# Performance work log

Hardware: AMD Instinct MI355X
Metric: run time of the kernel (lower is better)

## Reference

```python
import jax, jax.numpy as jnp
import numpy as np

EM_DIM = 64
GROUP = 16
DIM_IN = 1024


def _position_embedding(boxes, part_boxes):
    # boxes: [N,4], part_boxes: [P,4] -> [N,P,EM_DIM]
    xmin, ymin, xmax, ymax = [boxes[:, i:i + 1] for i in range(4)]            # [N,1]
    pxmin, pymin, pxmax, pymax = [part_boxes[:, i:i + 1].T for i in range(4)]  # [1,P]
    bw = xmax - xmin + 1.0
    bh = ymax - ymin + 1.0
    pw = pxmax - pxmin + 1.0
    ph = pymax - pymin + 1.0
    cx = 0.5 * (xmin + xmax)
    cy = 0.5 * (ymin + ymax)
    pcx = 0.5 * (pxmin + pxmax)
    pcy = 0.5 * (pymin + pymax)
    dx = jnp.abs((cx - pcx) / bw)
    dy = jnp.abs((cy - pcy) / bh)
    dx = jnp.log(jnp.where(dx < 1e-3, 1e-3, dx))
    dy = jnp.log(jnp.where(dy < 1e-3, 1e-3, dy))
    dw = jnp.log(pw / bw)
    dh = jnp.log(ph / bh)
    pos = jnp.stack([dx, dy, dw, dh], axis=2)                                  # [N,P,4]
    em_range = jnp.arange(EM_DIM // 8, dtype=pos.dtype) / (EM_DIM // 8)        # [8]
    em_mat = jnp.power(jnp.asarray(1000.0, pos.dtype), em_range)               # [8]
    div = (100.0 * pos)[..., None] / em_mat                                    # [N,P,4,8]
    emb = jnp.concatenate([jnp.sin(div), jnp.cos(div)], axis=3)                # [N,P,4,16]
    return emb.reshape(pos.shape[0], pos.shape[1], EM_DIM)


def _single_relation(boxes, part_boxes, bf, pf, Wg_w, Wg_b, Wq_w, Wq_b, Wk_w, Wk_b, conv_w, conv_b):
    N = bf.shape[0]
    P = pf.shape[0]
    emb = _position_embedding(boxes, part_boxes)                               # [N,P,64]
    pos_feat = jax.nn.relu(emb @ Wg_w.T + Wg_b)                                # [N,P,G]
    att_weight = jnp.transpose(pos_feat, (0, 2, 1))                            # [N,G,P]
    q = (bf @ Wq_w.T + Wq_b).reshape(N, GROUP, EM_DIM)                         # [N,G,64]
    k = (pf @ Wk_w.T + Wk_b).reshape(P, GROUP, EM_DIM)                         # [P,G,64]
    att = jnp.einsum('ngd,pgd->ngp', q, k) * (1.0 / GROUP)                     # [N,G,P]
    att_weight = jnp.where(att_weight < 1e-6, 1e-6, att_weight)
    sm = jax.nn.softmax(jnp.log(att_weight) + att, axis=2)                     # [N,G,P]
    out = jnp.einsum('ngp,pc->ngc', sm, pf)                                    # [N,G,dim_in]
    # grouped 1x1 conv: group g maps dim_in channels -> EM_DIM channels
    w3 = conv_w.reshape(GROUP, EM_DIM, DIM_IN)
    rel = jnp.einsum('ngc,goc->ngo', out, w3).reshape(N, GROUP * EM_DIM) + conv_b
    return rel                                                                  # [N, G*EM_DIM]


def setup_inputs() -> dict:
    key = jax.random.key(0)
    ks = jax.random.split(key, 12)
    N_TOT, P_TOT = 2048, 2048

    def make_rois(k1, k2, n, n1):
        xy = jax.random.uniform(k1, (n, 2), jnp.float32) * 800.0
        wh = jax.random.uniform(k2, (n, 2), jnp.float32) * 200.0 + 16.0
        boxes = jnp.concatenate([xy, xy + wh], axis=1)
        idx = jnp.concatenate([jnp.zeros((n1, 1)), jnp.ones((n - n1, 1))], axis=0).astype(jnp.float32)
        return jnp.concatenate([idx, boxes], axis=1)

    rois = make_rois(ks[0], ks[1], N_TOT, 1024)
    part_rois = make_rois(ks[2], ks[3], P_TOT, 1024)
    box_feats = jax.random.normal(ks[4], (N_TOT, DIM_IN), jnp.float32)
    part_feats = jax.random.normal(ks[5], (P_TOT, DIM_IN), jnp.float32)
    xav_g = float(np.sqrt(6.0 / (EM_DIM + GROUP)))
    xav_qk = float(np.sqrt(6.0 / (DIM_IN + GROUP * EM_DIM)))
    Wg_w = jax.random.uniform(ks[6], (GROUP, EM_DIM), jnp.float32, -xav_g, xav_g)
    Wg_b = jnp.zeros((GROUP,), jnp.float32)
    Wq_w = jax.random.uniform(ks[7], (GROUP * EM_DIM, DIM_IN), jnp.float32, -xav_qk, xav_qk)
    Wq_b = jnp.zeros((GROUP * EM_DIM,), jnp.float32)
    Wk_w = jax.random.uniform(ks[8], (GROUP * EM_DIM, DIM_IN), jnp.float32, -xav_qk, xav_qk)
    Wk_b = jnp.zeros((GROUP * EM_DIM,), jnp.float32)
    conv_w = jax.random.normal(ks[9], (GROUP * EM_DIM, DIM_IN), jnp.float32) * 0.02
    conv_b = jnp.zeros((GROUP * EM_DIM,), jnp.float32)
    return {"rois": rois, "part_rois": part_rois, "box_feats": box_feats,
            "part_feats": part_feats, "Wg_w": Wg_w, "Wg_b": Wg_b,
            "Wq_w": Wq_w, "Wq_b": Wq_b, "Wk_w": Wk_w, "Wk_b": Wk_b,
            "conv_w": conv_w, "conv_b": conv_b, "n1_boxes": 1024, "n1_parts": 1024}


def reference(rois, part_rois, box_feats, part_feats, Wg_w, Wg_b, Wq_w, Wq_b,
              Wk_w, Wk_b, conv_w, conv_b, n1_boxes, n1_parts):
    boxes = rois[:, 1:5]
    part_boxes = part_rois[:, 1:5]
    params = (Wg_w, Wg_b, Wq_w, Wq_b, Wk_w, Wk_b, conv_w, conv_b)
    rel1 = _single_relation(boxes[:n1_boxes], part_boxes[:n1_parts],
                            box_feats[:n1_boxes], part_feats[:n1_parts], *params)
    rel2 = _single_relation(boxes[n1_boxes:], part_boxes[n1_parts:],
                            box_feats[n1_boxes:], part_feats[n1_parts:], *params)
    return jnp.concatenate([rel1, rel2], axis=0)  # [N_total, GROUP*EM_DIM]
```

## Files before the change

kernel.cpp:

```cpp
#include <hip/hip_runtime.h>

typedef unsigned short u16;
using short8  = __attribute__((ext_vector_type(8))) short;
using float4v = __attribute__((ext_vector_type(4))) float;

__device__ __forceinline__ u16 f2bf(float f) {
    union { float f; unsigned u; } v; v.f = f;
    unsigned r = (v.u + 0x7fff + ((v.u >> 16) & 1)) >> 16;
    return (u16)r;
}
__device__ __forceinline__ float bf2f(u16 h) {
    union { unsigned u; float f; } v; v.u = ((unsigned)h) << 16; return v.f;
}
__device__ __forceinline__ unsigned pkbf(float lo, float hi) {
    unsigned d;
    asm("v_cvt_pk_bf16_f32 %0, %1, %2" : "=v"(d) : "v"(lo), "v"(hi));
    return d;
}
__device__ __forceinline__ float sin_rev(float r) {
    float f, s;
    asm("v_fract_f32 %0, %1" : "=v"(f) : "v"(r));
    asm("v_sin_f32 %0, %1" : "=v"(s) : "v"(f));
    return s;
}
__device__ __forceinline__ void dma16(const void* g, void* l) {
    __builtin_amdgcn_global_load_lds((const __attribute__((address_space(1))) void*)g,
                                     (__attribute__((address_space(3))) void*)l, 16, 0, 0);
}

__device__ __forceinline__ void cvt4(const float* __restrict__ s, u16* __restrict__ o, int i) {
    float4 v = ((const float4*)s)[i];
    uint2 r; r.x = pkbf(v.x, v.y); r.y = pkbf(v.z, v.w);
    ((uint2*)o)[i] = r;
}

__global__ __launch_bounds__(256)
void cvt_all(const float* __restrict__ s0, const float* __restrict__ s1,
             const float* __restrict__ s2, const float* __restrict__ s3,
             const float* __restrict__ s4, const float* __restrict__ prois,
             u16* __restrict__ o0, u16* __restrict__ o1, u16* __restrict__ o2,
             u16* __restrict__ o3, u16* __restrict__ o4, float4* __restrict__ PD,
             int na4, int nb4, int nw4, int PT) {
    int i = blockIdx.x * 256 + threadIdx.x;
    if (i < na4) { cvt4(s0, o0, i); return; }
    i -= na4;
    if (i < nb4) { cvt4(s1, o1, i); return; }
    i -= nb4;
    if (i < nw4) { cvt4(s2, o2, i); return; }
    i -= nw4;
    if (i < nw4) { cvt4(s3, o3, i); return; }
    i -= nw4;
    if (i < nw4) { cvt4(s4, o4, i); return; }
    i -= nw4;
    if (i < PT) {
        const float* pr = prois + (size_t)i * 5;
        float pxmin = pr[1], pymin = pr[2], pxmax = pr[3], pymax = pr[4];
        PD[i] = make_float4(0.5f * (pxmin + pxmax), 0.5f * (pymin + pymax),
                            __logf(pxmax - pxmin + 1.0f), __logf(pymax - pymin + 1.0f));
    }
}

__global__ __launch_bounds__(256)
void proj_mfma(const u16* __restrict__ Ab, const u16* __restrict__ Pb,
               const u16* __restrict__ Wqb, const u16* __restrict__ Wkb,
               const u16* __restrict__ Cwb, const float* __restrict__ bq,
               const float* __restrict__ bk, u16* __restrict__ Qb,
               u16* __restrict__ Kb, u16* __restrict__ PVt, int PT) {
    __shared__ __align__(16) u16 As[128 * 64];
    __shared__ __align__(16) u16 Ws[64 * 64];
    __shared__ __align__(16) u16 Tr[128 * 68];

    const int z = blockIdx.z;
    const int m0 = blockIdx.y * 128, j0 = blockIdx.x * 64;
    const u16* A = (z == 0) ? Ab : Pb;
    const u16* W = (z == 0) ? Wqb : (z == 1 ? Wkb : Cwb);
    const int t = threadIdx.x;
    const int w = t >> 6, lane = t & 63;
    const int wm = w >> 1, wn = w & 1;
    const int lr = lane >> 3, lc = lane & 7, gch = lc ^ lr;
    const int fm = lane & 15, quad = lane >> 4;

    float4v zero4 = {0.f, 0.f, 0.f, 0.f};
    float4v acc[4][2];
#pragma unroll
    for (int i = 0; i < 4; ++i) { acc[i][0] = zero4; acc[i][1] = zero4; }

    for (int k0 = 0; k0 < 1024; k0 += 64) {
#pragma unroll
        for (int i = 0; i < 4; ++i) {
            int row = w * 32 + i * 8 + lr;
            dma16(A + (size_t)(m0 + row) * 1024 + k0 + gch * 8,
                  As + (w * 32 + i * 8) * 64 + lane * 8);
        }
#pragma unroll
        for (int i = 0; i < 2; ++i) {
            int row = w * 16 + i * 8 + lr;
            dma16(W + (size_t)(j0 + row) * 1024 + k0 + gch * 8,
                  Ws + (w * 16 + i * 8) * 64 + lane * 8);
        }
        __syncthreads();
#pragma unroll
        for (int ks = 0; ks < 2; ++ks) {
            int c = ks * 4 + quad;
            short8 af[4], bf[2];
#pragma unroll
            for (int i = 0; i < 4; ++i) {
                int ra = wm * 64 + i * 16 + fm;
                af[i] = *(const short8*)(As + ra * 64 + ((c ^ (ra & 7)) * 8));
            }
#pragma unroll
            for (int j = 0; j < 2; ++j) {
                int rb = wn * 32 + j * 16 + fm;
                bf[j] = *(const short8*)(Ws + rb * 64 + ((c ^ (rb & 7)) * 8));
            }
#pragma unroll
            for (int i = 0; i < 4; ++i)
#pragma unroll
                for (int j = 0; j < 2; ++j)
                    acc[i][j] = __builtin_amdgcn_mfma_f32_16x16x32_bf16(af[i], bf[j], acc[i][j], 0, 0, 0);
        }
        __syncthreads();
    }

    if (z < 2) {
        u16* O = z ? Kb : Qb;
        const float* bias = z ? bk : bq;
#pragma unroll
        for (int j = 0; j < 2; ++j) {
            int jl = wn * 32 + j * 16 + fm;
            float bb = bias[j0 + jl];
#pragma unroll
            for (int i = 0; i < 4; ++i) {
                int mlb = wm * 64 + i * 16 + quad * 4;
#pragma unroll
                for (int r = 0; r < 4; ++r)
                    Tr[(mlb + r) * 68 + jl] = f2bf(acc[i][j][r] + bb);
            }
        }
        __syncthreads();
#pragma unroll
        for (int i2 = 0; i2 < 4; ++i2) {
            int f = i2 * 2048 + t * 8;
            int ml = f >> 6, jl = f & 63;
            union { uint2 u2[2]; short8 s8; } uu;
            uu.u2[0] = *(const uint2*)(Tr + ml * 68 + jl);
            uu.u2[1] = *(const uint2*)(Tr + ml * 68 + jl + 4);
            *(short8*)(O + (size_t)(m0 + ml) * 1024 + j0 + jl) = uu.s8;
        }
    } else {
#pragma unroll
        for (int j = 0; j < 2; ++j) {
            int jl = wn * 32 + j * 16 + fm;
#pragma unroll
            for (int i = 0; i < 4; ++i) {
                int mlb = wm * 64 + i * 16 + quad * 4;
                uint2 pk;
                pk.x = pkbf(acc[i][j][0], acc[i][j][1]);
                pk.y = pkbf(acc[i][j][2], acc[i][j][3]);
                *(uint2*)(Tr + jl * 136 + mlb) = pk;
            }
        }
        __syncthreads();
#pragma unroll
        for (int i2 = 0; i2 < 4; ++i2) {
            int f = i2 * 2048 + t * 8;
            int jl = f >> 7, ml = f & 127;
            union { uint2 u2[2]; short8 s8; } uu;
            uu.u2[0] = *(const uint2*)(Tr + jl * 136 + ml);
            uu.u2[1] = *(const uint2*)(Tr + jl * 136 + ml + 4);
            *(short8*)(PVt + (size_t)(j0 + jl) * PT + m0 + ml) = uu.s8;
        }
    }
}

__global__ __launch_bounds__(256)
void att_mfma(const u16* __restrict__ Qb, const u16* __restrict__ Kb,
              u16* __restrict__ ATT, const int* __restrict__ n1b_p,
              const int* __restrict__ n1p_p, int PT) {
    __shared__ __align__(16) u16 Qs[128 * 64];
    __shared__ __align__(16) u16 Ks[128 * 64];
    __shared__ __align__(16) u16 Tr[128 * 130];

    const int g = blockIdx.z;
    const int n0 = blockIdx.y * 128, pl0 = blockIdx.x * 128;
    const int n1b = *n1b_p, n1p = *n1p_p;
    const int hh = (n0 >= n1b) ? 1 : 0;
    const int p0 = hh ? n1p : 0;
    const int Ph = hh ? (PT - n1p) : n1p;
    if (pl0 >= Ph) return;
    const int t = threadIdx.x;
    const int w = t >> 6, lane = t & 63;
    const int wm = w >> 1, wn = w & 1;
    const int lr = lane >> 3, lc = lane & 7, gch = lc ^ lr;
    const int fm = lane & 15, quad = lane >> 4;

    float4v zero4 = {0.f, 0.f, 0.f, 0.f};
    float4v acc[4][4];
#pragma unroll
    for (int i = 0; i < 4; ++i)
#pragma unroll
        for (int j = 0; j < 4; ++j) acc[i][j] = zero4;

#pragma unroll
    for (int i = 0; i < 4; ++i) {
        int row = w * 32 + i * 8 + lr;
        dma16(Qb + (size_t)(n0 + row) * 1024 + g * 64 + gch * 8,
              Qs + (w * 32 + i * 8) * 64 + lane * 8);
        dma16(Kb + (size_t)(p0 + pl0 + row) * 1024 + g * 64 + gch * 8,
              Ks + (w * 32 + i * 8) * 64 + lane * 8);
    }
    __syncthreads();
#pragma unroll
    for (int ks = 0; ks < 2; ++ks) {
        int c = ks * 4 + quad;
        short8 af[4], bf[4];
#pragma unroll
        for (int i = 0; i < 4; ++i) {
            int ra = wm * 64 + i * 16 + fm;
            af[i] = *(const short8*)(Qs + ra * 64 + ((c ^ (ra & 7)) * 8));
            int rb = wn * 64 + i * 16 + fm;
            bf[i] = *(const short8*)(Ks + rb * 64 + ((c ^ (rb & 7)) * 8));
        }
#pragma unroll
        for (int i = 0; i < 4; ++i)
#pragma unroll
            for (int j = 0; j < 4; ++j)
                acc[i][j] = __builtin_amdgcn_mfma_f32_16x16x32_bf16(af[i], bf[j], acc[i][j], 0, 0, 0);
    }
#pragma unroll
    for (int j = 0; j < 4; ++j) {
        int pl = wn * 64 + j * 16 + fm;
#pragma unroll
        for (int i = 0; i < 4; ++i)
#pragma unroll
            for (int r = 0; r < 4; ++r) {
                int nl = wm * 64 + i * 16 + quad * 4 + r;
                Tr[nl * 130 + pl] = f2bf(__expf(acc[i][j][r] * 0.0625f));
            }
    }
    __syncthreads();
#pragma unroll
    for (int i = 0; i < 8; ++i) {
        int f = i * 2048 + t * 8;
        int nl = f >> 7, pl = f & 127;
        short8 v = *(const short8*)(Tr + nl * 130 + pl);
        *(short8*)(ATT + ((size_t)(n0 + nl) * 16 + g) * 1024 + pl0 + pl) = v;
    }
}

__global__ __launch_bounds__(256)
void softmax_fused(const float* __restrict__ rois, const float4* __restrict__ PD,
                   const float* __restrict__ Wg_w, const float* __restrict__ Wg_b,
                   u16* __restrict__ ATT, float* __restrict__ INV,
                   const int* __restrict__ n1b_p, const int* __restrict__ n1p_p, int PT) {
    __shared__ float redl[4][16];

    const int n = blockIdx.x, t = threadIdx.x;
    const int w = t >> 6, lane = t & 63;
    const int fm = lane & 15, quad = lane >> 4;
    const int n1b = *n1b_p, n1p = *n1p_p;
    const int hh = (n >= n1b) ? 1 : 0;
    const int p0 = hh ? n1p : 0;
    const int Ph = hh ? (PT - n1p) : n1p;

    float xmin = rois[n * 5 + 1], ymin = rois[n * 5 + 2];
    float xmax = rois[n * 5 + 3], ymax = rois[n * 5 + 4];
    float bw = xmax - xmin + 1.0f, bh = ymax - ymin + 1.0f;
    float cx = 0.5f * (xmin + xmax), cy = 0.5f * (ymin + ymax);

    const int jA = quad >> 1, trig = quad & 1;
    float cA   = (jA == 0) ? cx : cy;
    float invA = (jA == 0) ? (1.0f / bw) : (1.0f / bh);
    float lB   = (jA == 0) ? __logf(bw) : __logf(bh);
    float toff = trig ? 0.25f : 0.0f;

    const int g_ = fm;
    short8 b1, b2;
    {
        const float* w1 = Wg_w + g_ * 64 + quad * 8;
        const float* w2 = Wg_w + g_ * 64 + 32 + quad * 8;
        unsigned* p1 = (unsigned*)&b1;
        unsigned* p2 = (unsigned*)&b2;
#pragma unroll
        for (int kk = 0; kk < 4; ++kk) {
            p1[kk] = pkbf(w1[2 * kk], w1[2 * kk + 1]);
            p2[kk] = pkbf(w2[2 * kk], w2[2 * kk + 1]);
        }
    }
    float wgb = Wg_b[g_];

    const float inv_em[8] = {1.0f, 0.4216965034f, 0.1778279410f, 0.0749894209f,
                             0.0316227766f, 0.0133352143f, 0.0056234133f, 0.0023713737f};
    const float REV = 15.91549431f;
    const int prange = Ph >> 2;
    const int pb0 = w * prange;
    float ssum = 0.0f;
    u16* rowp = ATT + ((size_t)n * 16 + g_) * 1024;

    float4 pd_c = PD[p0 + pb0 + fm];
    ushort4 ea_c = *(const ushort4*)(rowp + pb0 + quad * 4);

#pragma unroll 2
    for (int pt = 0; pt < 16; ++pt) {
        int pbase = pb0 + pt * 16;
        float4 pd_n;
        ushort4 ea_n;
        if (pt < 15) {
            pd_n = PD[p0 + pbase + 16 + fm];
            ea_n = *(const ushort4*)(rowp + pbase + 16 + quad * 4);
        }
        float pc = (jA == 0) ? pd_c.x : pd_c.y;
        float lp = (jA == 0) ? pd_c.z : pd_c.w;
        float posA = __logf(fmaxf(fabsf(cA - pc) * invA, 0.001f));
        float posB = lp - lB;
        float br1 = posA * REV, br2 = posB * REV;
        float e1[8], e2[8];
#pragma unroll
        for (int k = 0; k < 8; ++k) {
            e1[k] = sin_rev(fmaf(br1, inv_em[k], toff));
            e2[k] = sin_rev(fmaf(br2, inv_em[k], toff));
        }
        short8 a1, a2;
        unsigned* pa1 = (unsigned*)&a1;
        unsigned* pa2 = (unsigned*)&a2;
#pragma unroll
        for (int kk = 0; kk < 4; ++kk) {
            pa1[kk] = pkbf(e1[2 * kk], e1[2 * kk + 1]);
            pa2[kk] = pkbf(e2[2 * kk], e2[2 * kk + 1]);
        }
        float4v acc = {wgb, wgb, wgb, wgb};
        acc = __builtin_amdgcn_mfma_f32_16x16x32_bf16(a1, b1, acc, 0, 0, 0);
        acc = __builtin_amdgcn_mfma_f32_16x16x32_bf16(a2, b2, acc, 0, 0, 0);

        float w0  = fmaxf(acc[0], 1e-6f) * bf2f(ea_c.x);
        float w1v = fmaxf(acc[1], 1e-6f) * bf2f(ea_c.y);
        float w2v = fmaxf(acc[2], 1e-6f) * bf2f(ea_c.z);
        float w3v = fmaxf(acc[3], 1e-6f) * bf2f(ea_c.w);
        ssum += (w0 + w1v) + (w2v + w3v);
        uint2 wp; wp.x = pkbf(w0, w1v); wp.y = pkbf(w2v, w3v);
        *(uint2*)(rowp + pbase + quad * 4) = wp;

        pd_c = pd_n;
        ea_c = ea_n;
    }

    ssum += __shfl_xor(ssum, 16, 64);
    ssum += __shfl_xor(ssum, 32, 64);
    if (lane < 16) redl[w][lane] = ssum;
    __syncthreads();
    if (t < 16)
        INV[(size_t)n * 16 + t] = 1.0f / (redl[0][t] + redl[1][t] + redl[2][t] + redl[3][t]);
}

__global__ __launch_bounds__(256)
void rel_mfma(const u16* __restrict__ SM, const u16* __restrict__ PVt,
              const float* __restrict__ conv_b, const float* __restrict__ INV,
              float* __restrict__ OUT, const int* __restrict__ n1b_p,
              const int* __restrict__ n1p_p, int PT) {
    __shared__ __align__(16) u16 As[64 * 64];
    __shared__ __align__(16) u16 Bs[64 * 64];

    const int n0 = blockIdx.x * 64, g = blockIdx.y;
    const int n1b = *n1b_p, n1p = *n1p_p;
    const int hh = (n0 >= n1b) ? 1 : 0;
    const int p0 = hh ? n1p : 0;
    const int Ph = hh ? (PT - n1p) : n1p;
    const int t = threadIdx.x;
    const int w = t >> 6, lane = t & 63;
    const int wm = w >> 1, wn = w & 1;
    const int lr = lane >> 3, lc = lane & 7, gch = lc ^ lr;
    const int fm = lane & 15, quad = lane >> 4;

    float4v zero4 = {0.f, 0.f, 0.f, 0.f};
    float4v acc[2][2];
#pragma unroll
    for (int i = 0; i < 2; ++i) { acc[i][0] = zero4; acc[i][1] = zero4; }

    for (int k0 = 0; k0 < Ph; k0 += 64) {
#pragma unroll
        for (int i = 0; i < 2; ++i) {
            int row = w * 16 + i * 8 + lr;
            dma16(SM + ((size_t)(n0 + row) * 16 + g) * 1024 + k0 + gch * 8,
                  As + (w * 16 + i * 8) * 64 + lane * 8);
            dma16(PVt + (size_t)(g * 64 + row) * PT + p0 + k0 + gch * 8,
                  Bs + (w * 16 + i * 8) * 64 + lane * 8);
        }
        __syncthreads();
#pragma unroll
        for (int ks = 0; ks < 2; ++ks) {
            int c = ks * 4 + quad;
            short8 af[2], bf[2];
#pragma unroll
            for (int i = 0; i < 2; ++i) {
                int ra = wm * 32 + i * 16 + fm;
                af[i] = *(const short8*)(As + ra * 64 + ((c ^ (ra & 7)) * 8));
                int rb = wn * 32 + i * 16 + fm;
                bf[i] = *(const short8*)(Bs + rb * 64 + ((c ^ (rb & 7)) * 8));
            }
#pragma unroll
            for (int i = 0; i < 2; ++i)
#pragma unroll
                for (int j = 0; j < 2; ++j)
                    acc[i][j] = __builtin_amdgcn_mfma_f32_16x16x32_bf16(af[i], bf[j], acc[i][j], 0, 0, 0);
        }
        __syncthreads();
    }
    float bb[2];
    bb[0] = conv_b[g * 64 + wn * 32 + fm];
    bb[1] = conv_b[g * 64 + wn * 32 + 16 + fm];
#pragma unroll
    for (int i = 0; i < 2; ++i)
#pragma unroll
        for (int r = 0; r < 4; ++r) {
            int nn = n0 + wm * 32 + i * 16 + quad * 4 + r;
            float iv = INV[(size_t)nn * 16 + g];
#pragma unroll
            for (int j = 0; j < 2; ++j) {
                int o = wn * 32 + j * 16 + fm;
                OUT[(size_t)nn * 1024 + g * 64 + o] = acc[i][j][r] * iv + bb[j];
            }
        }
}

extern "C" void kernel_launch(void* const* d_in, const int* in_sizes, int n_in,
                              void* d_out, int out_size, void* d_ws, size_t ws_size,
                              hipStream_t stream) {
    const float* rois   = (const float*)d_in[0];
    const float* prois  = (const float*)d_in[1];
    const float* bfeat  = (const float*)d_in[2];
    const float* pfeat  = (const float*)d_in[3];
    const float* Wg_w   = (const float*)d_in[4];
    const float* Wg_b   = (const float*)d_in[5];
    const float* Wq_w   = (const float*)d_in[6];
    const float* Wq_b   = (const float*)d_in[7];
    const float* Wk_w   = (const float*)d_in[8];
    const float* Wk_b   = (const float*)d_in[9];
    const float* conv_w = (const float*)d_in[10];
    const float* conv_b = (const float*)d_in[11];
    const int*   n1b    = (const int*)d_in[12];
    const int*   n1p    = (const int*)d_in[13];

    const int NT = in_sizes[2] / 1024;
    const int PT = in_sizes[3] / 1024;

    u16* ATT = (u16*)d_ws;
    u16* Qb  = ATT + (size_t)NT * 16 * 1024;
    u16* Kb  = Qb + (size_t)NT * 1024;
    u16* PVt = Kb + (size_t)PT * 1024;
    float* INVp = (float*)(PVt + (size_t)1024 * PT);
    float4* PD  = (float4*)(INVp + (size_t)NT * 16);
    u16* Ab  = ATT;
    u16* Pb  = Ab + (size_t)NT * 1024;
    u16* Wqb = Pb + (size_t)PT * 1024;
    u16* Wkb = Wqb + 1024 * 1024;
    u16* Cwb = Wkb + 1024 * 1024;

    dim3 blk(256);
    int nf4 = NT * 1024 / 4, pf4 = PT * 1024 / 4, wf4 = 1024 * 1024 / 4;
    int tot = nf4 + pf4 + 3 * wf4 + PT;
    cvt_all<<<dim3((tot + 255) / 256), blk, 0, stream>>>(
        bfeat, pfeat, Wq_w, Wk_w, conv_w, prois, Ab, Pb, Wqb, Wkb, Cwb, PD,
        nf4, pf4, wf4, PT);

    proj_mfma<<<dim3(16, NT / 128, 3), blk, 0, stream>>>(Ab, Pb, Wqb, Wkb, Cwb,
                                                         Wq_b, Wk_b, Qb, Kb, PVt, PT);
    att_mfma<<<dim3(PT / 128, NT / 128, 16), blk, 0, stream>>>(Qb, Kb, ATT, n1b, n1p, PT);
    softmax_fused<<<dim3(NT), blk, 0, stream>>>(rois, PD, Wg_w, Wg_b, ATT, INVp, n1b, n1p, PT);
    rel_mfma<<<dim3(NT / 64, 16), blk, 0, stream>>>(ATT, PVt, conv_b, INVp,
                                                    (float*)d_out, n1b, n1p, PT);
}
```

Measured before the change: 203.9 us.

## Fuse QK attention logits into relation GEMM, flash-style with position weights

```diff
diff --git a/kernel.cpp b/kernel.cpp
--- a/kernel.cpp
+++ b/kernel.cpp
@@ -174,87 +174,10 @@
 }
 
 __global__ __launch_bounds__(256)
-void att_mfma(const u16* __restrict__ Qb, const u16* __restrict__ Kb,
-              u16* __restrict__ ATT, const int* __restrict__ n1b_p,
-              const int* __restrict__ n1p_p, int PT) {
-    __shared__ __align__(16) u16 Qs[128 * 64];
-    __shared__ __align__(16) u16 Ks[128 * 64];
-    __shared__ __align__(16) u16 Tr[128 * 130];
-
-    const int g = blockIdx.z;
-    const int n0 = blockIdx.y * 128, pl0 = blockIdx.x * 128;
-    const int n1b = *n1b_p, n1p = *n1p_p;
-    const int hh = (n0 >= n1b) ? 1 : 0;
-    const int p0 = hh ? n1p : 0;
-    const int Ph = hh ? (PT - n1p) : n1p;
-    if (pl0 >= Ph) return;
-    const int t = threadIdx.x;
-    const int w = t >> 6, lane = t & 63;
-    const int wm = w >> 1, wn = w & 1;
-    const int lr = lane >> 3, lc = lane & 7, gch = lc ^ lr;
-    const int fm = lane & 15, quad = lane >> 4;
-
-    float4v zero4 = {0.f, 0.f, 0.f, 0.f};
-    float4v acc[4][4];
-#pragma unroll
-    for (int i = 0; i < 4; ++i)
-#pragma unroll
-        for (int j = 0; j < 4; ++j) acc[i][j] = zero4;
-
-#pragma unroll
-    for (int i = 0; i < 4; ++i) {
-        int row = w * 32 + i * 8 + lr;
-        dma16(Qb + (size_t)(n0 + row) * 1024 + g * 64 + gch * 8,
-              Qs + (w * 32 + i * 8) * 64 + lane * 8);
-        dma16(Kb + (size_t)(p0 + pl0 + row) * 1024 + g * 64 + gch * 8,
-              Ks + (w * 32 + i * 8) * 64 + lane * 8);
-    }
-    __syncthreads();
-#pragma unroll
-    for (int ks = 0; ks < 2; ++ks) {
-        int c = ks * 4 + quad;
-        short8 af[4], bf[4];
-#pragma unroll
-        for (int i = 0; i < 4; ++i) {
-            int ra = wm * 64 + i * 16 + fm;
-            af[i] = *(const short8*)(Qs + ra * 64 + ((c ^ (ra & 7)) * 8));
-            int rb = wn * 64 + i * 16 + fm;
-            bf[i] = *(const short8*)(Ks + rb * 64 + ((c ^ (rb & 7)) * 8));
-        }
-#pragma unroll
-        for (int i = 0; i < 4; ++i)
-#pragma unroll
-            for (int j = 0; j < 4; ++j)
-                acc[i][j] = __builtin_amdgcn_mfma_f32_16x16x32_bf16(af[i], bf[j], acc[i][j], 0, 0, 0);
-    }
-#pragma unroll
-    for (int j = 0; j < 4; ++j) {
-        int pl = wn * 64 + j * 16 + fm;
-#pragma unroll
-        for (int i = 0; i < 4; ++i)
-#pragma unroll
-            for (int r = 0; r < 4; ++r) {
-                int nl = wm * 64 + i * 16 + quad * 4 + r;
-                Tr[nl * 130 + pl] = f2bf(__expf(acc[i][j][r] * 0.0625f));
-            }
-    }
-    __syncthreads();
-#pragma unroll
-    for (int i = 0; i < 8; ++i) {
-        int f = i * 2048 + t * 8;
-        int nl = f >> 7, pl = f & 127;
-        short8 v = *(const short8*)(Tr + nl * 130 + pl);
-        *(short8*)(ATT + ((size_t)(n0 + nl) * 16 + g) * 1024 + pl0 + pl) = v;
-    }
-}
-
-__global__ __launch_bounds__(256)
-void softmax_fused(const float* __restrict__ rois, const float4* __restrict__ PD,
-                   const float* __restrict__ Wg_w, const float* __restrict__ Wg_b,
-                   u16* __restrict__ ATT, float* __restrict__ INV,
-                   const int* __restrict__ n1b_p, const int* __restrict__ n1p_p, int PT) {
-    __shared__ float redl[4][16];
-
+void posw_fused(const float* __restrict__ rois, const float4* __restrict__ PD,
+                const float* __restrict__ Wg_w, const float* __restrict__ Wg_b,
+                u16* __restrict__ POSW, const int* __restrict__ n1b_p,
+                const int* __restrict__ n1p_p, int PT) {
     const int n = blockIdx.x, t = threadIdx.x;
     const int w = t >> 6, lane = t & 63;
     const int fm = lane & 15, quad = lane >> 4;
@@ -294,21 +217,15 @@
     const float REV = 15.91549431f;
     const int prange = Ph >> 2;
     const int pb0 = w * prange;
-    float ssum = 0.0f;
-    u16* rowp = ATT + ((size_t)n * 16 + g_) * 1024;
+    u16* rowp = POSW + ((size_t)n * 16 + g_) * 1024;
 
     float4 pd_c = PD[p0 + pb0 + fm];
-    ushort4 ea_c = *(const ushort4*)(rowp + pb0 + quad * 4);
 
 #pragma unroll 2
     for (int pt = 0; pt < 16; ++pt) {
         int pbase = pb0 + pt * 16;
         float4 pd_n;
-        ushort4 ea_n;
-        if (pt < 15) {
-            pd_n = PD[p0 + pbase + 16 + fm];
-            ea_n = *(const ushort4*)(rowp + pbase + 16 + quad * 4);
-        }
+        if (pt < 15) pd_n = PD[p0 + pbase + 16 + fm];
         float pc = (jA == 0) ? pd_c.x : pd_c.y;
         float lp = (jA == 0) ? pd_c.z : pd_c.w;
         float posA = __logf(fmaxf(fabsf(cA - pc) * invA, 0.001f));
@@ -332,33 +249,28 @@
         acc = __builtin_amdgcn_mfma_f32_16x16x32_bf16(a1, b1, acc, 0, 0, 0);
         acc = __builtin_amdgcn_mfma_f32_16x16x32_bf16(a2, b2, acc, 0, 0, 0);
 
-        float w0  = fmaxf(acc[0], 1e-6f) * bf2f(ea_c.x);
-        float w1v = fmaxf(acc[1], 1e-6f) * bf2f(ea_c.y);
-        float w2v = fmaxf(acc[2], 1e-6f) * bf2f(ea_c.z);
-        float w3v = fmaxf(acc[3], 1e-6f) * bf2f(ea_c.w);
-        ssum += (w0 + w1v) + (w2v + w3v);
+        float w0  = fmaxf(acc[0], 1e-6f);
+        float w1v = fmaxf(acc[1], 1e-6f);
+        float w2v = fmaxf(acc[2], 1e-6f);
+        float w3v = fmaxf(acc[3], 1e-6f);
         uint2 wp; wp.x = pkbf(w0, w1v); wp.y = pkbf(w2v, w3v);
         *(uint2*)(rowp + pbase + quad * 4) = wp;
 
         pd_c = pd_n;
-        ea_c = ea_n;
-    }
-
-    ssum += __shfl_xor(ssum, 16, 64);
-    ssum += __shfl_xor(ssum, 32, 64);
-    if (lane < 16) redl[w][lane] = ssum;
-    __syncthreads();
-    if (t < 16)
-        INV[(size_t)n * 16 + t] = 1.0f / (redl[0][t] + redl[1][t] + redl[2][t] + redl[3][t]);
+    }
 }
 
 __global__ __launch_bounds__(256)
-void rel_mfma(const u16* __restrict__ SM, const u16* __restrict__ PVt,
-              const float* __restrict__ conv_b, const float* __restrict__ INV,
-              float* __restrict__ OUT, const int* __restrict__ n1b_p,
-              const int* __restrict__ n1p_p, int PT) {
-    __shared__ __align__(16) u16 As[64 * 64];
-    __shared__ __align__(16) u16 Bs[64 * 64];
+void fused_rel(const u16* __restrict__ Qb, const u16* __restrict__ Kb,
+               const u16* __restrict__ POSW, const u16* __restrict__ PVt,
+               const float* __restrict__ conv_b, float* __restrict__ OUT,
+               const int* __restrict__ n1b_p, const int* __restrict__ n1p_p, int PT) {
+    __shared__ __align__(16) u16 Qs[64 * 64];
+    __shared__ __align__(16) u16 Ks[64 * 64];
+    __shared__ __align__(16) u16 Ps[64 * 64];
+    __shared__ __align__(16) u16 Vs[64 * 64];
+    __shared__ __align__(16) u16 Wt[64 * 64];
+    __shared__ float redl[2][64];
 
     const int n0 = blockIdx.x * 64, g = blockIdx.y;
     const int n1b = *n1b_p, n1p = *n1p_p;
@@ -371,40 +283,135 @@
     const int lr = lane >> 3, lc = lane & 7, gch = lc ^ lr;
     const int fm = lane & 15, quad = lane >> 4;
 
+#pragma unroll
+    for (int i = 0; i < 2; ++i) {
+        int row = w * 16 + i * 8 + lr;
+        dma16(Qb + (size_t)(n0 + row) * 1024 + g * 64 + gch * 8,
+              Qs + (w * 16 + i * 8) * 64 + lane * 8);
+        dma16(Kb + (size_t)(p0 + row) * 1024 + g * 64 + gch * 8,
+              Ks + (w * 16 + i * 8) * 64 + lane * 8);
+        dma16(POSW + ((size_t)(n0 + row) * 16 + g) * 1024 + gch * 8,
+              Ps + (w * 16 + i * 8) * 64 + lane * 8);
+    }
+
     float4v zero4 = {0.f, 0.f, 0.f, 0.f};
-    float4v acc[2][2];
-#pragma unroll
-    for (int i = 0; i < 2; ++i) { acc[i][0] = zero4; acc[i][1] = zero4; }
-
-    for (int k0 = 0; k0 < Ph; k0 += 64) {
+    float4v oacc[2][2];
+    float rsum[2][4];
+#pragma unroll
+    for (int i = 0; i < 2; ++i) {
+        oacc[i][0] = zero4; oacc[i][1] = zero4;
+#pragma unroll
+        for (int r = 0; r < 4; ++r) rsum[i][r] = 0.f;
+    }
+
+    __syncthreads();
+
+    short8 qf[2][2];
+#pragma unroll
+    for (int ks = 0; ks < 2; ++ks) {
+        int c = ks * 4 + quad;
+#pragma unroll
+        for (int i = 0; i < 2; ++i) {
+            int ra = wm * 32 + i * 16 + fm;
+            qf[ks][i] = *(const short8*)(Qs + ra * 64 + ((c ^ (ra & 7)) * 8));
+        }
+    }
+
+    const int NPT = Ph >> 6;
+    for (int pt = 0; pt < NPT; ++pt) {
 #pragma unroll
         for (int i = 0; i < 2; ++i) {
             int row = w * 16 + i * 8 + lr;
-            dma16(SM + ((size_t)(n0 + row) * 16 + g) * 1024 + k0 + gch * 8,
-                  As + (w * 16 + i * 8) * 64 + lane * 8);
-            dma16(PVt + (size_t)(g * 64 + row) * PT + p0 + k0 + gch * 8,
-                  Bs + (w * 16 + i * 8) * 64 + lane * 8);
-        }
-        __syncthreads();
+            dma16(PVt + (size_t)(g * 64 + row) * PT + p0 + pt * 64 + gch * 8,
+                  Vs + (w * 16 + i * 8) * 64 + lane * 8);
+        }
+        float4v atc[2][2];
+        atc[0][0] = zero4; atc[0][1] = zero4; atc[1][0] = zero4; atc[1][1] = zero4;
 #pragma unroll
         for (int ks = 0; ks < 2; ++ks) {
             int c = ks * 4 + quad;
-            short8 af[2], bf[2];
+            short8 bfr[2];
+#pragma unroll
+            for (int j = 0; j < 2; ++j) {
+                int rb = wn * 32 + j * 16 + fm;
+                bfr[j] = *(const short8*)(Ks + rb * 64 + ((c ^ (rb & 7)) * 8));
+            }
+#pragma unroll
+            for (int i = 0; i < 2; ++i)
+#pragma unroll
+                for (int j = 0; j < 2; ++j)
+                    atc[i][j] = __builtin_amdgcn_mfma_f32_16x16x32_bf16(qf[ks][i], bfr[j], atc[i][j], 0, 0, 0);
+        }
+#pragma unroll
+        for (int j = 0; j < 2; ++j) {
+            int pl = wn * 32 + j * 16 + fm;
+            int pch = pl >> 3, psub = pl & 7;
+#pragma unroll
+            for (int i = 0; i < 2; ++i)
+#pragma unroll
+                for (int r = 0; r < 4; ++r) {
+                    int nl = wm * 32 + i * 16 + quad * 4 + r;
+                    int sw = ((pch ^ (nl & 7)) * 8) + psub;
+                    float pw = bf2f(Ps[nl * 64 + sw]);
+                    float wv = pw * __expf(atc[i][j][r] * 0.0625f);
+                    rsum[i][r] += wv;
+                    Wt[nl * 64 + sw] = f2bf(wv);
+                }
+        }
+        __syncthreads();
+        if (pt + 1 < NPT) {
+#pragma unroll
+            for (int i = 0; i < 2; ++i) {
+                int row = w * 16 + i * 8 + lr;
+                dma16(Kb + (size_t)(p0 + (pt + 1) * 64 + row) * 1024 + g * 64 + gch * 8,
+                      Ks + (w * 16 + i * 8) * 64 + lane * 8);
+                dma16(POSW + ((size_t)(n0 + row) * 16 + g) * 1024 + (pt + 1) * 64 + gch * 8,
+                      Ps + (w * 16 + i * 8) * 64 + lane * 8);
+            }
+        }
+#pragma unroll
+        for (int ks = 0; ks < 2; ++ks) {
+            int c = ks * 4 + quad;
+            short8 wf[2], vf[2];
 #pragma unroll
             for (int i = 0; i < 2; ++i) {
                 int ra = wm * 32 + i * 16 + fm;
-                af[i] = *(const short8*)(As + ra * 64 + ((c ^ (ra & 7)) * 8));
-                int rb = wn * 32 + i * 16 + fm;
-                bf[i] = *(const short8*)(Bs + rb * 64 + ((c ^ (rb & 7)) * 8));
+                wf[i] = *(const short8*)(Wt + ra * 64 + ((c ^ (ra & 7)) * 8));
+            }
+#pragma unroll
+            for (int j = 0; j < 2; ++j) {
+                int rb = wn * 32 + j * 16 + fm;
+                vf[j] = *(const short8*)(Vs + rb * 64 + ((c ^ (rb & 7)) * 8));
             }
 #pragma unroll
             for (int i = 0; i < 2; ++i)
 #pragma unroll
                 for (int j = 0; j < 2; ++j)
-                    acc[i][j] = __builtin_amdgcn_mfma_f32_16x16x32_bf16(af[i], bf[j], acc[i][j], 0, 0, 0);
-        }
-        __syncthreads();
-    }
+                    oacc[i][j] = __builtin_amdgcn_mfma_f32_16x16x32_bf16(wf[i], vf[j], oacc[i][j], 0, 0, 0);
+        }
+        __syncthreads();
+    }
+
+#pragma unroll
+    for (int i = 0; i < 2; ++i)
+#pragma unroll
+        for (int r = 0; r < 4; ++r) {
+            float s = rsum[i][r];
+            s += __shfl_xor(s, 1, 64);
+            s += __shfl_xor(s, 2, 64);
+            s += __shfl_xor(s, 4, 64);
+            s += __shfl_xor(s, 8, 64);
+            rsum[i][r] = s;
+        }
+    if (fm == 0) {
+#pragma unroll
+        for (int i = 0; i < 2; ++i)
+#pragma unroll
+            for (int r = 0; r < 4; ++r)
+                redl[wn][wm * 32 + i * 16 + quad * 4 + r] = rsum[i][r];
+    }
+    __syncthreads();
+
     float bb[2];
     bb[0] = conv_b[g * 64 + wn * 32 + fm];
     bb[1] = conv_b[g * 64 + wn * 32 + 16 + fm];
@@ -412,12 +419,12 @@
     for (int i = 0; i < 2; ++i)
 #pragma unroll
         for (int r = 0; r < 4; ++r) {
-            int nn = n0 + wm * 32 + i * 16 + quad * 4 + r;
-            float iv = INV[(size_t)nn * 16 + g];
+            int nl = wm * 32 + i * 16 + quad * 4 + r;
+            float inv = 1.0f / (redl[0][nl] + redl[1][nl]);
 #pragma unroll
             for (int j = 0; j < 2; ++j) {
                 int o = wn * 32 + j * 16 + fm;
-                OUT[(size_t)nn * 1024 + g * 64 + o] = acc[i][j][r] * iv + bb[j];
+                OUT[(size_t)(n0 + nl) * 1024 + g * 64 + o] = oacc[i][j][r] * inv + bb[j];
             }
         }
 }
@@ -443,17 +450,16 @@
     const int NT = in_sizes[2] / 1024;
     const int PT = in_sizes[3] / 1024;
 
-    u16* ATT = (u16*)d_ws;
-    u16* Qb  = ATT + (size_t)NT * 16 * 1024;
-    u16* Kb  = Qb + (size_t)NT * 1024;
-    u16* PVt = Kb + (size_t)PT * 1024;
-    float* INVp = (float*)(PVt + (size_t)1024 * PT);
-    float4* PD  = (float4*)(INVp + (size_t)NT * 16);
-    u16* Ab  = ATT;
-    u16* Pb  = Ab + (size_t)NT * 1024;
-    u16* Wqb = Pb + (size_t)PT * 1024;
-    u16* Wkb = Wqb + 1024 * 1024;
-    u16* Cwb = Wkb + 1024 * 1024;
+    u16* Qb   = (u16*)d_ws;
+    u16* Kb   = Qb + (size_t)NT * 1024;
+    u16* PVt  = Kb + (size_t)PT * 1024;
+    float4* PD = (float4*)(PVt + (size_t)1024 * PT);
+    u16* POSW = (u16*)(PD + PT);
+    u16* Ab   = POSW + (size_t)NT * 16 * 1024;
+    u16* Pb   = Ab + (size_t)NT * 1024;
+    u16* Wqb  = Pb + (size_t)PT * 1024;
+    u16* Wkb  = Wqb + 1024 * 1024;
+    u16* Cwb  = Wkb + 1024 * 1024;
 
     dim3 blk(256);
     int nf4 = NT * 1024 / 4, pf4 = PT * 1024 / 4, wf4 = 1024 * 1024 / 4;
@@ -464,8 +470,7 @@
 
     proj_mfma<<<dim3(16, NT / 128, 3), blk, 0, stream>>>(Ab, Pb, Wqb, Wkb, Cwb,
                                                          Wq_b, Wk_b, Qb, Kb, PVt, PT);
-    att_mfma<<<dim3(PT / 128, NT / 128, 16), blk, 0, stream>>>(Qb, Kb, ATT, n1b, n1p, PT);
-    softmax_fused<<<dim3(NT), blk, 0, stream>>>(rois, PD, Wg_w, Wg_b, ATT, INVp, n1b, n1p, PT);
-    rel_mfma<<<dim3(NT / 64, 16), blk, 0, stream>>>(ATT, PVt, conv_b, INVp,
-                                                    (float*)d_out, n1b, n1p, PT);
-}
+    posw_fused<<<dim3(NT), blk, 0, stream>>>(rois, PD, Wg_w, Wg_b, POSW, n1b, n1p, PT);
+    fused_rel<<<dim3(NT / 64, 16), blk, 0, stream>>>(Qb, Kb, POSW, PVt, conv_b,
+                                                     (float*)d_out, n1b, n1p, PT);
+}
```

New measurement: 178.2 us. 12.6% less time.
